# Optimization experiments

Measured on AMD Instinct MI355X. Metric: run time of the kernel, lower is better.

Reference implementation:

```python
import jax, jax.numpy as jnp
import numpy as np

B, N, C, F, E, K = 4, 4096, 1024, 4096, 8, 2

def setup_inputs() -> dict:
    key = jax.random.key(0)
    ks = jax.random.split(key, 6)
    x = jax.random.normal(ks[0], (B, N, C), dtype=jnp.float32)
    router_w = jax.random.normal(ks[1], (E, C), dtype=jnp.float32) * 0.02  # nn.Linear weight [out,in]
    w1 = jax.random.normal(ks[2], (E, C, F), dtype=jnp.float32) * (1.0 / np.sqrt(C))
    b1 = jnp.zeros((E, F), dtype=jnp.float32)
    w2 = jax.random.normal(ks[3], (E, F, C), dtype=jnp.float32) * (1.0 / np.sqrt(F))
    b2 = jnp.zeros((E, C), dtype=jnp.float32)
    return {"x": x, "router_w": router_w, "w1": w1, "b1": b1, "w2": w2, "b2": b2}

def reference(x, router_w, w1, b1, w2, b2):
    Bx, Nx, Cx = x.shape
    xf = x.reshape(-1, Cx)                                  # [T, C]
    logits = xf @ router_w.T                                # [T, E]
    probs = jax.nn.softmax(logits, axis=-1)
    top_w, top_i = jax.lax.top_k(probs, K)                  # [T, K]
    top_w = top_w / (jnp.sum(top_w, axis=-1, keepdims=True) + 1e-9)
    out = jnp.zeros_like(xf)
    for e in range(E):
        # combine weight for expert e per token (0 if not routed)
        gate = jnp.sum(jnp.where(top_i == e, top_w, 0.0), axis=-1)   # [T]
        h = jax.nn.gelu(xf @ w1[e] + b1[e], approximate=False)       # [T, F]
        y = h @ w2[e] + b2[e]                                        # [T, C]
        out = out + gate[:, None] * y
    return out.reshape(Bx, Nx, Cx)
```

## Files before the change

### kernel.cpp

```cpp
#include <hip/hip_runtime.h>
#include <hip/hip_fp16.h>

#define T_TOK 16384
#define C_DIM 1024
#define F_DIM 4096
#define E_NUM 8

typedef _Float16 half8 __attribute__((ext_vector_type(8)));
typedef _Float16 half4v __attribute__((ext_vector_type(4)));
typedef float f32x4 __attribute__((ext_vector_type(4)));

static constexpr size_t META_OFF  = 0;
static constexpr size_t XB_OFF    = 256;
static constexpr size_t W1T_OFF   = XB_OFF  + (size_t)2*T_TOK*C_DIM;
static constexpr size_t W2T_OFF   = W1T_OFF + (size_t)2*E_NUM*C_DIM*F_DIM;
static constexpr size_t HB_OFF    = W2T_OFF + (size_t)2*E_NUM*C_DIM*F_DIM;
static constexpr size_t YB_OFF    = HB_OFF  + (size_t)2*T_TOK*2*F_DIM;
static constexpr size_t TOK_OFF   = YB_OFF  + (size_t)2*T_TOK*2*C_DIM;
static constexpr size_t GATE_OFF  = TOK_OFF + (size_t)4*E_NUM*T_TOK;
static constexpr size_t TSLOT_OFF = GATE_OFF+ (size_t)4*E_NUM*T_TOK;
static constexpr size_t EPAIR_OFF = TSLOT_OFF + (size_t)4*T_TOK*2;
static constexpr size_t GPAIR_OFF = EPAIR_OFF + (size_t)4*T_TOK;
static constexpr size_t WS_NEED   = GPAIR_OFF + (size_t)8*T_TOK;

__device__ __forceinline__ void async16(void* lds, const void* g) {
  __builtin_amdgcn_global_load_lds((const __attribute__((address_space(1))) unsigned int*)g,
                                   (__attribute__((address_space(3))) unsigned int*)lds,
                                   16, 0, 0);
}

__global__ __launch_bounds__(256) void transpose_cast_kernel(const float* __restrict__ in,
                                                             _Float16* __restrict__ outp,
                                                             int R, int Cc) {
  __shared__ float tile[64][65];
  int e = blockIdx.z;
  const float* ip = in + (size_t)e * R * Cc;
  _Float16* op = outp + (size_t)e * R * Cc;
  int c0 = blockIdx.x * 64, r0 = blockIdx.y * 64;
  int tid = threadIdx.x;
  int lr = tid >> 4, lc = (tid & 15) * 4;
  #pragma unroll
  for (int d = 0; d < 4; ++d) {
    int row = lr + d * 16;
    float4 v = *(const float4*)(ip + (size_t)(r0 + row) * Cc + c0 + lc);
    tile[row][lc]     = v.x;
    tile[row][lc + 1] = v.y;
    tile[row][lc + 2] = v.z;
    tile[row][lc + 3] = v.w;
  }
  __syncthreads();
  int oc = tid >> 3, or8 = (tid & 7) * 8;
  #pragma unroll
  for (int d = 0; d < 2; ++d) {
    int c = oc + d * 32;
    half8 h;
    #pragma unroll
    for (int j = 0; j < 8; ++j) h[j] = (_Float16)tile[or8 + j][c];
    *(half8*)(op + (size_t)(c0 + c) * R + r0 + or8) = h;
  }
}

__global__ __launch_bounds__(256) void router_kernel(const float* __restrict__ x,
                                                     const float* __restrict__ rw,
                                                     int* __restrict__ epair,
                                                     float2* __restrict__ gpair,
                                                     _Float16* __restrict__ xb) {
  int wv = threadIdx.x >> 6, l = threadIdx.x & 63;
  int t = blockIdx.x * 4 + wv;
  const float* xr = x + (size_t)t * C_DIM;
  double acc[E_NUM] = {};
  #pragma unroll
  for (int j = 0; j < 4; ++j) {
    float4 xv = *(const float4*)(xr + j * 256 + l * 4);
    half4v hv;
    hv[0] = (_Float16)xv.x; hv[1] = (_Float16)xv.y;
    hv[2] = (_Float16)xv.z; hv[3] = (_Float16)xv.w;
    *(half4v*)(xb + (size_t)t * C_DIM + j * 256 + l * 4) = hv;
    #pragma unroll
    for (int e = 0; e < E_NUM; ++e) {
      float4 w4 = *(const float4*)(rw + (size_t)e * C_DIM + j * 256 + l * 4);
      acc[e] += (double)xv.x * w4.x + (double)xv.y * w4.y +
                (double)xv.z * w4.z + (double)xv.w * w4.w;
    }
  }
  #pragma unroll
  for (int e = 0; e < E_NUM; ++e)
    #pragma unroll
    for (int off = 32; off; off >>= 1)
      acc[e] += __shfl_xor(acc[e], off, 64);

  if (l == 0) {
    double m = acc[0];
    #pragma unroll
    for (int e = 1; e < E_NUM; ++e) m = acc[e] > m ? acc[e] : m;
    double p[E_NUM], s = 0.0;
    #pragma unroll
    for (int e = 0; e < E_NUM; ++e) { p[e] = exp(acc[e] - m); s += p[e]; }
    int i0 = 0; double b0 = p[0];
    #pragma unroll
    for (int e = 1; e < E_NUM; ++e) if (p[e] > b0) { b0 = p[e]; i0 = e; }
    int i1 = -1; double b1v = -1.0;
    #pragma unroll
    for (int e = 0; e < E_NUM; ++e) if (e != i0 && p[e] > b1v) { b1v = p[e]; i1 = e; }
    double q0 = b0 / s, q1 = b1v / s;
    double den = q0 + q1 + 1e-9;
    epair[t] = i0 | (i1 << 8);
    gpair[t] = make_float2((float)(q0 / den), (float)(q1 / den));
  }
}

__global__ __launch_bounds__(1024) void assign_kernel(const int* __restrict__ epair,
                                                      const float2* __restrict__ gpair,
                                                      int* __restrict__ counts,
                                                      int* __restrict__ tok,
                                                      float* __restrict__ gate,
                                                      int* __restrict__ tslot) {
  __shared__ int wsum[16];
  __shared__ int wbase[16];
  __shared__ int stot;
  int myE = blockIdx.x;
  int tid = threadIdx.x, wid = tid >> 6, lane = tid & 63;
  int base = 0;
  for (int it = 0; it < (T_TOK * 2) / 1024; ++it) {
    int idx = it * 1024 + tid;
    int t = idx >> 1, k = idx & 1;
    int ep = epair[t];
    int e = (k ? (ep >> 8) : ep) & 0xff;
    bool f = (e == myE);
    unsigned long long mask = __ballot(f);
    int lanep = __popcll(mask & ((1ull << lane) - 1ull));
    if (lane == 0) wsum[wid] = __popcll(mask);
    __syncthreads();
    if (tid == 0) {
      int s = 0;
      #pragma unroll
      for (int i = 0; i < 16; ++i) { wbase[i] = s; s += wsum[i]; }
      stot = s;
    }
    __syncthreads();
    if (f) {
      int slot = base + wbase[wid] + lanep;
      float2 g = gpair[t];
      tok[myE * T_TOK + slot] = t;
      gate[myE * T_TOK + slot] = k ? g.y : g.x;
      tslot[idx] = (myE << 24) | slot;
    }
    base += stot;
  }
  if (tid == 0) counts[myE] = base;
}

__global__ void plan_kernel(int* meta) {
  if (threadIdx.x == 0 && blockIdx.x == 0) {
    int ro = 0, to = 0;
    meta[8] = 0; meta[17] = 0;
    for (int e = 0; e < E_NUM; ++e) {
      int c = meta[e];
      ro += c; to += (c + 127) >> 7;
      meta[9 + e] = ro; meta[18 + e] = to;
    }
  }
}


__global__ __launch_bounds__(256) void gemm1_kernel(const _Float16* __restrict__ xb,
                                                    const _Float16* __restrict__ w1t,
                                                    const float* __restrict__ b1,
                                                    _Float16* __restrict__ hbuf,
                                                    const int* __restrict__ tok,
                                                    const int* __restrict__ meta) {
  __shared__ _Float16 smem[8192];
  __shared__ int tokLds[128];

  int bid = blockIdx.x;
  int swz = (bid & 7) * 1056 + (bid >> 3);
  int band = swz >> 8, rem = swz & 255;
  int nt = rem >> 3;
  int mt = band * 8 + (rem & 7);
  if (mt >= meta[17 + E_NUM]) return;
  int e = 0;
  while (mt >= meta[18 + e]) ++e;
  int ne = meta[e];
  int r0 = (mt - meta[17 + e]) << 7;
  int valid = ne - r0; if (valid > 128) valid = 128;

  int tid = threadIdx.x;
  if (tid < 128) {
    int r = tid < valid ? tid : valid - 1;
    tokLds[tid] = tok[e * T_TOK + r0 + r];
  }
  __syncthreads();

  int row = tid >> 2, c4 = tid & 3;
  int ch = c4 ^ ((row >> 1) & 3);
  const _Float16* aSrc0 = xb + (size_t)tokLds[row] * C_DIM + ch * 8;
  const _Float16* aSrc1 = xb + (size_t)tokLds[row + 64] * C_DIM + ch * 8;
  const _Float16* bSrc0 = w1t + ((size_t)e * F_DIM + nt * 128 + row) * C_DIM + ch * 8;
  const _Float16* bSrc1 = bSrc0 + (size_t)64 * C_DIM;

  char* SM = (char*)smem;
  char* dst = SM + (size_t)tid * 16;

  int w = tid >> 6, l = tid & 63;
  int wm = w >> 1, wn = w & 1;
  int rl = l & 15, q = l >> 4;
  int swq = (q ^ ((rl >> 1) & 3)) * 16;
  int aBy = wm * 4096 + rl * 64 + swq;
  int bBy = 8192 + wn * 4096 + rl * 64 + swq;

  f32x4 acc[4][4] = {};
  constexpr int NT = C_DIM / 32;
  for (int kt = 0; kt < NT; ++kt) {
    __syncthreads();
    int ko = kt * 32;
    async16(dst,          aSrc0 + ko);
    async16(dst + 4096,   aSrc1 + ko);
    async16(dst + 8192,   bSrc0 + ko);
    async16(dst + 12288,  bSrc1 + ko);
    __syncthreads();
    half8 af[4], bf[4];
    #pragma unroll
    for (int m = 0; m < 4; ++m)
      af[m] = *(const half8*)(SM + aBy + m * 1024);
    #pragma unroll
    for (int n = 0; n < 4; ++n)
      bf[n] = *(const half8*)(SM + bBy + n * 1024);
    #pragma unroll
    for (int m = 0; m < 4; ++m)
      #pragma unroll
      for (int n = 0; n < 4; ++n)
        acc[m][n] = __builtin_amdgcn_mfma_f32_16x16x32_f16(af[m], bf[n], acc[m][n], 0, 0, 0);
  }

  int hbase = meta[8 + e] + r0;
  float bv[4];
  #pragma unroll
  for (int n = 0; n < 4; ++n)
    bv[n] = b1[(size_t)e * F_DIM + nt * 128 + wn * 64 + n * 16 + rl];
  #pragma unroll
  for (int m = 0; m < 4; ++m) {
    int rb = wm * 64 + m * 16 + q * 4;
    #pragma unroll
    for (int n = 0; n < 4; ++n) {
      int col = nt * 128 + wn * 64 + n * 16 + rl;
      #pragma unroll
      for (int r = 0; r < 4; ++r) {
        int rr = rb + r;
        if (rr < valid) {
          float pre = acc[m][n][r] + bv[n];
          float g = 0.5f * pre * (1.0f + erff(pre * 0.70710678118654752f));
          hbuf[(size_t)(hbase + rr) * F_DIM + col] = (_Float16)g;
        }
      }
    }
  }
}

__global__ __launch_bounds__(256) void gemm2_kernel(const _Float16* __restrict__ hbuf,
                                                    const _Float16* __restrict__ w2t,
                                                    const float* __restrict__ b2,
                                                    _Float16* __restrict__ ybuf,
                                                    const float* __restrict__ gate,
                                                    const int* __restrict__ meta) {
  __shared__ _Float16 smem[8192];
  __shared__ float gateLds[128];

  int bid = blockIdx.x;
  int swz = (bid & 7) * 264 + (bid >> 3);
  int band = swz >> 6, rem = swz & 63;
  int nt = rem >> 3;
  int mt = band * 8 + (rem & 7);
  if (mt >= meta[17 + E_NUM]) return;
  int e = 0;
  while (mt >= meta[18 + e]) ++e;
  int ne = meta[e];
  int r0 = (mt - meta[17 + e]) << 7;
  int valid = ne - r0; if (valid > 128) valid = 128;
  int hbase = meta[8 + e] + r0;

  int tid = threadIdx.x;
  if (tid < 128) {
    int r = tid < valid ? tid : valid - 1;
    gateLds[tid] = gate[e * T_TOK + r0 + r];
  }
  __syncthreads();

  int row = tid >> 2, c4 = tid & 3;
  int ch = c4 ^ ((row >> 1) & 3);
  int rcA0 = row      < valid ? row      : valid - 1;
  int rcA1 = row + 64 < valid ? row + 64 : valid - 1;
  const _Float16* aSrc0 = hbuf + (size_t)(hbase + rcA0) * F_DIM + ch * 8;
  const _Float16* aSrc1 = hbuf + (size_t)(hbase + rcA1) * F_DIM + ch * 8;
  const _Float16* bSrc0 = w2t + ((size_t)e * C_DIM + nt * 128 + row) * F_DIM + ch * 8;
  const _Float16* bSrc1 = bSrc0 + (size_t)64 * F_DIM;

  char* SM = (char*)smem;
  char* dst = SM + (size_t)tid * 16;

  int w = tid >> 6, l = tid & 63;
  int wm = w >> 1, wn = w & 1;
  int rl = l & 15, q = l >> 4;
  int swq = (q ^ ((rl >> 1) & 3)) * 16;
  int aBy = wm * 4096 + rl * 64 + swq;
  int bBy = 8192 + wn * 4096 + rl * 64 + swq;

  f32x4 acc[4][4] = {};
  constexpr int NT = F_DIM / 32;
  for (int kt = 0; kt < NT; ++kt) {
    __syncthreads();
    int ko = kt * 32;
    async16(dst,          aSrc0 + ko);
    async16(dst + 4096,   aSrc1 + ko);
    async16(dst + 8192,   bSrc0 + ko);
    async16(dst + 12288,  bSrc1 + ko);
    __syncthreads();
    half8 af[4], bf[4];
    #pragma unroll
    for (int m = 0; m < 4; ++m)
      af[m] = *(const half8*)(SM + aBy + m * 1024);
    #pragma unroll
    for (int n = 0; n < 4; ++n)
      bf[n] = *(const half8*)(SM + bBy + n * 1024);
    #pragma unroll
    for (int m = 0; m < 4; ++m)
      #pragma unroll
      for (int n = 0; n < 4; ++n)
        acc[m][n] = __builtin_amdgcn_mfma_f32_16x16x32_f16(af[m], bf[n], acc[m][n], 0, 0, 0);
  }

  float bv[4];
  #pragma unroll
  for (int n = 0; n < 4; ++n)
    bv[n] = b2[(size_t)e * C_DIM + nt * 128 + wn * 64 + n * 16 + rl];
  #pragma unroll
  for (int m = 0; m < 4; ++m) {
    int rb = wm * 64 + m * 16 + q * 4;
    #pragma unroll
    for (int n = 0; n < 4; ++n) {
      int col = nt * 128 + wn * 64 + n * 16 + rl;
      #pragma unroll
      for (int r = 0; r < 4; ++r) {
        int rr = rb + r;
        if (rr < valid) {
          float val = gateLds[rr] * (acc[m][n][r] + bv[n]);
          ybuf[(size_t)(hbase + rr) * C_DIM + col] = (_Float16)val;
        }
      }
    }
  }
}

__global__ __launch_bounds__(256) void combine_kernel(const _Float16* __restrict__ ybuf,
                                                      const int* __restrict__ tslot,
                                                      const int* __restrict__ meta,
                                                      float* __restrict__ out) {
  int gid = blockIdx.x * 256 + threadIdx.x;
  int t = gid >> 7;
  int cc = (gid & 127) << 3;
  int s0 = tslot[t * 2], s1 = tslot[t * 2 + 1];
  size_t r0 = (size_t)meta[8 + (s0 >> 24)] + (s0 & 0xFFFFFF);
  size_t r1 = (size_t)meta[8 + (s1 >> 24)] + (s1 & 0xFFFFFF);
  half8 y0 = *(const half8*)(ybuf + r0 * C_DIM + cc);
  half8 y1 = *(const half8*)(ybuf + r1 * C_DIM + cc);
  float4 o0, o1;
  o0.x = (float)y0[0] + (float)y1[0];
  o0.y = (float)y0[1] + (float)y1[1];
  o0.z = (float)y0[2] + (float)y1[2];
  o0.w = (float)y0[3] + (float)y1[3];
  o1.x = (float)y0[4] + (float)y1[4];
  o1.y = (float)y0[5] + (float)y1[5];
  o1.z = (float)y0[6] + (float)y1[6];
  o1.w = (float)y0[7] + (float)y1[7];
  *(float4*)(out + (size_t)t * C_DIM + cc) = o0;
  *(float4*)(out + (size_t)t * C_DIM + cc + 4) = o1;
}

extern "C" void kernel_launch(void* const* d_in, const int* in_sizes, int n_in,
                              void* d_out, int out_size, void* d_ws, size_t ws_size,
                              hipStream_t stream) {
  (void)in_sizes; (void)n_in; (void)out_size;
  if (!d_ws || ws_size < WS_NEED) return;

  const float* x  = (const float*)d_in[0];
  const float* rw = (const float*)d_in[1];
  const float* w1 = (const float*)d_in[2];
  const float* b1 = (const float*)d_in[3];
  const float* w2 = (const float*)d_in[4];
  const float* b2 = (const float*)d_in[5];
  float* out = (float*)d_out;

  char* ws = (char*)d_ws;
  int*       meta  = (int*)(ws + META_OFF);
  _Float16*  xb    = (_Float16*)(ws + XB_OFF);
  _Float16*  w1t   = (_Float16*)(ws + W1T_OFF);
  _Float16*  w2t   = (_Float16*)(ws + W2T_OFF);
  _Float16*  hbuf  = (_Float16*)(ws + HB_OFF);
  _Float16*  ybuf  = (_Float16*)(ws + YB_OFF);
  int*       tok   = (int*)(ws + TOK_OFF);
  float*     gate  = (float*)(ws + GATE_OFF);
  int*       tslot = (int*)(ws + TSLOT_OFF);
  int*       epair = (int*)(ws + EPAIR_OFF);
  float2*    gpair = (float2*)(ws + GPAIR_OFF);

  hipMemsetAsync(meta, 0, 256, stream);

  transpose_cast_kernel<<<dim3(F_DIM / 64, C_DIM / 64, E_NUM), 256, 0, stream>>>(w1, w1t, C_DIM, F_DIM);
  transpose_cast_kernel<<<dim3(C_DIM / 64, F_DIM / 64, E_NUM), 256, 0, stream>>>(w2, w2t, F_DIM, C_DIM);
  router_kernel<<<T_TOK / 4, 256, 0, stream>>>(x, rw, epair, gpair, xb);
  assign_kernel<<<E_NUM, 1024, 0, stream>>>(epair, gpair, meta, tok, gate, tslot);
  plan_kernel<<<1, 64, 0, stream>>>(meta);

  gemm1_kernel<<<264 * 32, 256, 0, stream>>>(xb, w1t, b1, hbuf, tok, meta);
  gemm2_kernel<<<264 * 8, 256, 0, stream>>>(hbuf, w2t, b2, ybuf, gate, meta);
  combine_kernel<<<(T_TOK * (C_DIM / 8)) / 256, 256, 0, stream>>>(ybuf, tslot, meta, out);
}
```

Baseline: 1.004 ms.

## Double-buffer LDS tiles with BK=64 prefetch in both expert GEMMs

Both expert GEMM kernels now use a 64-wide K tile and two LDS buffers of 32KB each. The next tile's async global-to-LDS copies are issued before the MFMAs on the current tile, and there is one barrier per iteration instead of two. This is meant to hide global load latency behind compute and halve the barrier count. The cost is 64KB of LDS per block, which lowers occupancy, and the last iteration issues a redundant reload of the same tile.

```diff
diff --git a/kernel.cpp b/kernel.cpp
--- a/kernel.cpp
+++ b/kernel.cpp
@@ -169,7 +169,7 @@
                                                     _Float16* __restrict__ hbuf,
                                                     const int* __restrict__ tok,
                                                     const int* __restrict__ meta) {
-  __shared__ _Float16 smem[8192];
+  __shared__ _Float16 smem[32768];
   __shared__ int tokLds[128];
 
   int bid = blockIdx.x;
@@ -199,37 +199,51 @@
   const _Float16* bSrc1 = bSrc0 + (size_t)64 * C_DIM;
 
   char* SM = (char*)smem;
-  char* dst = SM + (size_t)tid * 16;
-
-  int w = tid >> 6, l = tid & 63;
-  int wm = w >> 1, wn = w & 1;
+
+  int w0 = tid >> 6, l = tid & 63;
+  int wm = w0 >> 1, wn = w0 & 1;
   int rl = l & 15, q = l >> 4;
   int swq = (q ^ ((rl >> 1) & 3)) * 16;
   int aBy = wm * 4096 + rl * 64 + swq;
-  int bBy = 8192 + wn * 4096 + rl * 64 + swq;
+  int bBy = 16384 + wn * 4096 + rl * 64 + swq;
+
+  {
+    char* d0 = SM + (size_t)tid * 16;
+    async16(d0,          aSrc0);      async16(d0 + 4096,  aSrc1);
+    async16(d0 + 8192,   aSrc0 + 32); async16(d0 + 12288, aSrc1 + 32);
+    async16(d0 + 16384,  bSrc0);      async16(d0 + 20480, bSrc1);
+    async16(d0 + 24576,  bSrc0 + 32); async16(d0 + 28672, bSrc1 + 32);
+  }
+  __syncthreads();
 
   f32x4 acc[4][4] = {};
-  constexpr int NT = C_DIM / 32;
+  constexpr int NT = C_DIM / 64;
+  int cur = 0;
   for (int kt = 0; kt < NT; ++kt) {
+    int kn = (kt + 1 < NT ? kt + 1 : kt) * 64;
+    char* dn = SM + (cur ^ 1) * 32768 + (size_t)tid * 16;
+    async16(dn,          aSrc0 + kn);      async16(dn + 4096,  aSrc1 + kn);
+    async16(dn + 8192,   aSrc0 + kn + 32); async16(dn + 12288, aSrc1 + kn + 32);
+    async16(dn + 16384,  bSrc0 + kn);      async16(dn + 20480, bSrc1 + kn);
+    async16(dn + 24576,  bSrc0 + kn + 32); async16(dn + 28672, bSrc1 + kn + 32);
+    const char* Tb = (const char*)SM + cur * 32768;
+    #pragma unroll
+    for (int ks = 0; ks < 2; ++ks) {
+      half8 af[4], bf[4];
+      #pragma unroll
+      for (int m = 0; m < 4; ++m)
+        af[m] = *(const half8*)(Tb + ks * 8192 + aBy + m * 1024);
+      #pragma unroll
+      for (int n = 0; n < 4; ++n)
+        bf[n] = *(const half8*)(Tb + ks * 8192 + bBy + n * 1024);
+      #pragma unroll
+      for (int m = 0; m < 4; ++m)
+        #pragma unroll
+        for (int n = 0; n < 4; ++n)
+          acc[m][n] = __builtin_amdgcn_mfma_f32_16x16x32_f16(af[m], bf[n], acc[m][n], 0, 0, 0);
+    }
     __syncthreads();
-    int ko = kt * 32;
-    async16(dst,          aSrc0 + ko);
-    async16(dst + 4096,   aSrc1 + ko);
-    async16(dst + 8192,   bSrc0 + ko);
-    async16(dst + 12288,  bSrc1 + ko);
-    __syncthreads();
-    half8 af[4], bf[4];
-    #pragma unroll
-    for (int m = 0; m < 4; ++m)
-      af[m] = *(const half8*)(SM + aBy + m * 1024);
-    #pragma unroll
-    for (int n = 0; n < 4; ++n)
-      bf[n] = *(const half8*)(SM + bBy + n * 1024);
-    #pragma unroll
-    for (int m = 0; m < 4; ++m)
-      #pragma unroll
-      for (int n = 0; n < 4; ++n)
-        acc[m][n] = __builtin_amdgcn_mfma_f32_16x16x32_f16(af[m], bf[n], acc[m][n], 0, 0, 0);
+    cur ^= 1;
   }
 
   int hbase = meta[8 + e] + r0;
@@ -262,7 +276,7 @@
                                                     _Float16* __restrict__ ybuf,
                                                     const float* __restrict__ gate,
                                                     const int* __restrict__ meta) {
-  __shared__ _Float16 smem[8192];
+  __shared__ _Float16 smem[32768];
   __shared__ float gateLds[128];
 
   int bid = blockIdx.x;
@@ -295,37 +309,51 @@
   const _Float16* bSrc1 = bSrc0 + (size_t)64 * F_DIM;
 
   char* SM = (char*)smem;
-  char* dst = SM + (size_t)tid * 16;
-
-  int w = tid >> 6, l = tid & 63;
-  int wm = w >> 1, wn = w & 1;
+
+  int w0 = tid >> 6, l = tid & 63;
+  int wm = w0 >> 1, wn = w0 & 1;
   int rl = l & 15, q = l >> 4;
   int swq = (q ^ ((rl >> 1) & 3)) * 16;
   int aBy = wm * 4096 + rl * 64 + swq;
-  int bBy = 8192 + wn * 4096 + rl * 64 + swq;
+  int bBy = 16384 + wn * 4096 + rl * 64 + swq;
+
+  {
+    char* d0 = SM + (size_t)tid * 16;
+    async16(d0,          aSrc0);      async16(d0 + 4096,  aSrc1);
+    async16(d0 + 8192,   aSrc0 + 32); async16(d0 + 12288, aSrc1 + 32);
+    async16(d0 + 16384,  bSrc0);      async16(d0 + 20480, bSrc1);
+    async16(d0 + 24576,  bSrc0 + 32); async16(d0 + 28672, bSrc1 + 32);
+  }
+  __syncthreads();
 
   f32x4 acc[4][4] = {};
-  constexpr int NT = F_DIM / 32;
+  constexpr int NT = F_DIM / 64;
+  int cur = 0;
   for (int kt = 0; kt < NT; ++kt) {
+    int kn = (kt + 1 < NT ? kt + 1 : kt) * 64;
+    char* dn = SM + (cur ^ 1) * 32768 + (size_t)tid * 16;
+    async16(dn,          aSrc0 + kn);      async16(dn + 4096,  aSrc1 + kn);
+    async16(dn + 8192,   aSrc0 + kn + 32); async16(dn + 12288, aSrc1 + kn + 32);
+    async16(dn + 16384,  bSrc0 + kn);      async16(dn + 20480, bSrc1 + kn);
+    async16(dn + 24576,  bSrc0 + kn + 32); async16(dn + 28672, bSrc1 + kn + 32);
+    const char* Tb = (const char*)SM + cur * 32768;
+    #pragma unroll
+    for (int ks = 0; ks < 2; ++ks) {
+      half8 af[4], bf[4];
+      #pragma unroll
+      for (int m = 0; m < 4; ++m)
+        af[m] = *(const half8*)(Tb + ks * 8192 + aBy + m * 1024);
+      #pragma unroll
+      for (int n = 0; n < 4; ++n)
+        bf[n] = *(const half8*)(Tb + ks * 8192 + bBy + n * 1024);
+      #pragma unroll
+      for (int m = 0; m < 4; ++m)
+        #pragma unroll
+        for (int n = 0; n < 4; ++n)
+          acc[m][n] = __builtin_amdgcn_mfma_f32_16x16x32_f16(af[m], bf[n], acc[m][n], 0, 0, 0);
+    }
     __syncthreads();
-    int ko = kt * 32;
-    async16(dst,          aSrc0 + ko);
-    async16(dst + 4096,   aSrc1 + ko);
-    async16(dst + 8192,   bSrc0 + ko);
-    async16(dst + 12288,  bSrc1 + ko);
-    __syncthreads();
-    half8 af[4], bf[4];
-    #pragma unroll
-    for (int m = 0; m < 4; ++m)
-      af[m] = *(const half8*)(SM + aBy + m * 1024);
-    #pragma unroll
-    for (int n = 0; n < 4; ++n)
-      bf[n] = *(const half8*)(SM + bBy + n * 1024);
-    #pragma unroll
-    for (int m = 0; m < 4; ++m)
-      #pragma unroll
-      for (int n = 0; n < 4; ++n)
-        acc[m][n] = __builtin_amdgcn_mfma_f32_16x16x32_f16(af[m], bf[n], acc[m][n], 0, 0, 0);
+    cur ^= 1;
   }
 
   float bv[4];
```

New measurement: 1.207 ms. +20.2%, slower.
